# Performance work log

Hardware: AMD Instinct MI355X
Metric: run time of the kernel (lower is better)

Reference implementation:

```python
import jax, jax.numpy as jnp
import numpy as np

N, E = 50000, 800000
H, C, K = 8, 16, 4
LAMBD = 1.0
DECAY = [float(np.log(LAMBD / (k + 1) + (1 + 1e-06))) for k in range(K + 1)]


def setup_inputs() -> dict:
    key = jax.random.key(0)
    ks = jax.random.split(key, 10)
    s = 0.05  # keep activations stable over K hops
    return {
        "x": jax.random.normal(ks[0], (N, 256), jnp.float32),
        "edge_index": jax.random.randint(ks[1], (2, E), 0, N, jnp.int64),
        "W0": jax.random.normal(ks[2], (256, 128), jnp.float32) * s,
        "b0": jnp.zeros((128,), jnp.float32),
        "W1": jax.random.normal(ks[3], (128, 128), jnp.float32) * s,
        "b1": jnp.zeros((128,), jnp.float32),
        "Wout": jax.random.normal(ks[4], (128, 40), jnp.float32) * s,
        "bout": jnp.zeros((40,), jnp.float32),
        "hop_att0": jax.random.normal(ks[5], (H, C), jnp.float32) * s,
        "hop_atts": jax.random.normal(ks[6], (K, H, 2 * C), jnp.float32) * s,
        "atts": jax.random.normal(ks[7], (K, H, C), jnp.float32) * s,
        "hop_biases": jnp.ones((K + 1, H), jnp.float32),
    }


def _aero_forward(x, edge_index, W0, b0, W1, b1, Wout, bout,
                  hop_att0, hop_atts, atts, hop_biases):
    n = x.shape[0]
    # add self loops (cached_edge_index is None in the torch module)
    loops = jnp.arange(n, dtype=edge_index.dtype)
    row = jnp.concatenate([edge_index[0], loops])  # source j
    col = jnp.concatenate([edge_index[1], loops])  # target i

    # hid_feat_init (dropout p=0 -> identity); num_layers=2
    h = x @ W0 + b0
    h = jax.nn.elu(h) @ W1 + b1
    h = h.reshape(n, H, C)

    # k = 0 hop attention
    g = jnp.einsum('hc,nhc->nh', hop_att0, jax.nn.elu(h)) + hop_biases[0]
    z = h * g[..., None]
    z_scale = z * DECAY[0]

    for k in range(1, K + 1):
        # edge attention: gather, elementwise, degree-normalize
        zi = z_scale[col]          # [E', H, C] target
        zj = z_scale[row]          # [E', H, C] source
        a = jnp.einsum('hc,ehc->eh', atts[k - 1], jax.nn.elu(zi + zj))
        a = jax.nn.softplus(a) + 1e-06                       # [E', H]
        deg = jax.ops.segment_sum(a, col, num_segments=n)    # [N, H]
        dinv = jnp.where(deg > 0, deg ** -0.5, 0.0)
        a = dinv[row] * a * dinv[col]
        # propagate: scatter-add weighted source features onto targets
        h = jax.ops.segment_sum(a[..., None] * h[row], col, num_segments=n)
        # hop attention on concat(h, z_scale)
        hz = jax.nn.elu(jnp.concatenate([h, z_scale], axis=-1))  # [N, H, 2C]
        g = jnp.einsum('hc,nhc->nh', hop_atts[k - 1], hz) + hop_biases[k]
        z = z + h * g[..., None]
        z_scale = z * DECAY[k]

    # node classifier
    z = jax.nn.elu(z.reshape(n, H * C))
    return z @ Wout + bout


def reference(x, edge_index, W0, b0, W1, b1, Wout, bout,
              hop_att0, hop_atts, atts, hop_biases):
    return _aero_forward(x, edge_index, W0, b0, W1, b1, Wout, bout,
                         hop_att0, hop_atts, atts, hop_biases)
```

## Files before the change

kernel.cpp:

```cpp
#include <hip/hip_runtime.h>
#include <hip/hip_fp16.h>
#include <math.h>

#define NH 8
#define NC 16
#define HC 128

typedef __attribute__((ext_vector_type(8))) _Float16 half8;
typedef __attribute__((ext_vector_type(4))) float f32x4;

__device__ __forceinline__ float eluf(float x) { return x > 0.f ? x : __expf(x) - 1.f; }
__device__ __forceinline__ float splusf(float x) { return fmaxf(x, 0.f) + __logf(1.f + __expf(-fabsf(x))); }

#if __has_builtin(__builtin_amdgcn_exp2f)
#define EXP2F(x) __builtin_amdgcn_exp2f(x)
#else
#define EXP2F(x) exp2f(x)
#endif

__global__ void count_kernel(const int* __restrict__ ei, int* __restrict__ cnt, int E, int E2) {
    int e = blockIdx.x * blockDim.x + threadIdx.x;
    if (e >= E2) return;
    int col = (e < E) ? ei[E + e] : (e - E);
    atomicAdd(&cnt[col], 1);
}

__global__ void scan1_kernel(const int* __restrict__ counts, int* __restrict__ ptr,
                             int* __restrict__ partials, int n) {
    __shared__ int tmp[256];
    int t = threadIdx.x;
    int i = blockIdx.x * 256 + t;
    int v = (i < n) ? counts[i] : 0;
    tmp[t] = v;
    __syncthreads();
    for (int off = 1; off < 256; off <<= 1) {
        int add = (t >= off) ? tmp[t - off] : 0;
        __syncthreads();
        tmp[t] += add;
        __syncthreads();
    }
    if (i < n) ptr[i] = tmp[t] - v;
    if (t == 255) partials[blockIdx.x] = tmp[255];
}

__global__ void scan2_kernel(int* __restrict__ partials, int nb) {
    __shared__ int tmp[256];
    int t = threadIdx.x;
    int v = (t < nb) ? partials[t] : 0;
    tmp[t] = v;
    __syncthreads();
    for (int off = 1; off < 256; off <<= 1) {
        int add = (t >= off) ? tmp[t - off] : 0;
        __syncthreads();
        tmp[t] += add;
        __syncthreads();
    }
    if (t < nb) partials[t] = tmp[t] - v;
}

__global__ void scan3_kernel(int* __restrict__ ptr, const int* __restrict__ partials,
                             int n, int total) {
    int i = blockIdx.x * 256 + threadIdx.x;
    if (i < n) ptr[i] += partials[blockIdx.x];
    if (i == 0) ptr[n] = total;
}

__global__ void fill_kernel(const int* __restrict__ ei, const int* __restrict__ ptr,
                            int* __restrict__ cursor, int* __restrict__ src, int E, int E2) {
    int e = blockIdx.x * blockDim.x + threadIdx.x;
    if (e >= E2) return;
    int col, row;
    if (e < E) { row = ei[e]; col = ei[E + e]; }
    else       { row = e - E; col = e - E; }
    int pos = ptr[col] + atomicAdd(&cursor[col], 1);
    src[pos] = row;
}

__global__ void wswz_kernel(const float* __restrict__ W, _Float16* __restrict__ Wf, int NKS) {
    int t = blockIdx.x * 256 + threadIdx.x;
    if (t >= 8 * NKS * 64) return;
    int lane = t & 63;
    int ks = (t >> 6) % NKS;
    int cg = (t >> 6) / NKS;
    int n = cg * 16 + (lane & 15);
    int k0 = ks * 32 + (lane >> 4) * 8;
    half8 v;
#pragma unroll
    for (int j = 0; j < 8; ++j) v[j] = (_Float16)W[(size_t)(k0 + j) * 128 + n];
    *(half8*)(Wf + (size_t)t * 8) = v;
}

template<int K, bool A16, bool HOP0>
__global__ __launch_bounds__(256)
void mfma_gemm(const float* __restrict__ A32, const _Float16* __restrict__ A16p,
               const _Float16* __restrict__ Wf, const float* __restrict__ bias,
               int M, _Float16* __restrict__ h1_out,
               float* __restrict__ z_out, _Float16* __restrict__ h16_out,
               _Float16* __restrict__ z16_out,
               const float* __restrict__ att0, const float* __restrict__ hb0) {
    constexpr int NKS = K / 32;
    __shared__ float sL[64 * 132];
    const int tid = threadIdx.x;
    const int w = tid >> 6;
    const int lane = tid & 63;
    const int l15 = lane & 15;
    const int lg = lane >> 4;
    const int m0 = blockIdx.x * 64;

    f32x4 acc[4][2];
#pragma unroll
    for (int a = 0; a < 4; ++a)
#pragma unroll
        for (int b = 0; b < 2; ++b)
            acc[a][b] = f32x4{0.f, 0.f, 0.f, 0.f};

#pragma unroll
    for (int ks = 0; ks < NKS; ++ks) {
        const int kb = ks * 32 + lg * 8;
        half8 af[4];
        if (A16) {
#pragma unroll
            for (int mf = 0; mf < 4; ++mf) {
                int row = m0 + mf * 16 + l15;
                af[mf] = *(const half8*)(A16p + ((size_t)row << 7) + kb);
            }
        } else {
#pragma unroll
            for (int mf = 0; mf < 4; ++mf) {
                int row = m0 + mf * 16 + l15;
                float4 a0 = make_float4(0.f, 0.f, 0.f, 0.f), a1 = a0;
                if (row < M) {
                    const float* ap = A32 + (size_t)row * K + kb;
                    a0 = *(const float4*)ap;
                    a1 = *(const float4*)(ap + 4);
                }
                half8 h;
                h[0] = (_Float16)a0.x; h[1] = (_Float16)a0.y;
                h[2] = (_Float16)a0.z; h[3] = (_Float16)a0.w;
                h[4] = (_Float16)a1.x; h[5] = (_Float16)a1.y;
                h[6] = (_Float16)a1.z; h[7] = (_Float16)a1.w;
                af[mf] = h;
            }
        }
        half8 bf[2];
#pragma unroll
        for (int cf = 0; cf < 2; ++cf) {
            int cg = w * 2 + cf;
            bf[cf] = *(const half8*)(Wf + (size_t)((cg * NKS + ks) * 64 + lane) * 8);
        }
#pragma unroll
        for (int mf = 0; mf < 4; ++mf)
#pragma unroll
            for (int cf = 0; cf < 2; ++cf)
                acc[mf][cf] = __builtin_amdgcn_mfma_f32_16x16x32_f16(af[mf], bf[cf],
                                                                     acc[mf][cf], 0, 0, 0);
    }

#pragma unroll
    for (int mf = 0; mf < 4; ++mf)
#pragma unroll
        for (int cf = 0; cf < 2; ++cf) {
            int col = w * 32 + cf * 16 + l15;
#pragma unroll
            for (int r = 0; r < 4; ++r)
                sL[(mf * 16 + lg * 4 + r) * 132 + col] = acc[mf][cf][r];
        }
    __syncthreads();

    const int rr = lane;
    const int q = w;
    const int row = m0 + rr;
    float v[32];
#pragma unroll
    for (int t = 0; t < 8; ++t)
        *(float4*)&v[t * 4] = *(const float4*)&sL[rr * 132 + q * 32 + t * 4];
#pragma unroll
    for (int t = 0; t < 8; ++t) {
        float4 bv = *(const float4*)&bias[q * 32 + t * 4];
        v[t * 4 + 0] += bv.x; v[t * 4 + 1] += bv.y;
        v[t * 4 + 2] += bv.z; v[t * 4 + 3] += bv.w;
    }

    if (!HOP0) {
        if (row < M) {
            half8 o[4];
#pragma unroll
            for (int c = 0; c < 32; ++c) o[c >> 3][c & 7] = (_Float16)eluf(v[c]);
            _Float16* hp = h1_out + ((size_t)row << 7) + q * 32;
#pragma unroll
            for (int t = 0; t < 4; ++t) *(half8*)(hp + t * 8) = o[t];
        }
    } else {
        float g[2];
#pragma unroll
        for (int hh = 0; hh < 2; ++hh) {
            int head = q * 2 + hh;
            float p = 0.f;
#pragma unroll
            for (int c = 0; c < 16; ++c)
                p = fmaf(att0[head * 16 + c], eluf(v[hh * 16 + c]), p);
            g[hh] = p + hb0[head];
        }
        if (row < M) {
            float zz[32];
#pragma unroll
            for (int c = 0; c < 32; ++c) zz[c] = v[c] * g[c >> 4];
            half8 ho[4], zo[4];
#pragma unroll
            for (int c = 0; c < 32; ++c) {
                ho[c >> 3][c & 7] = (_Float16)v[c];
                zo[c >> 3][c & 7] = (_Float16)zz[c];
            }
            _Float16* hp  = h16_out + ((size_t)row << 7) + q * 32;
            _Float16* zhp = z16_out + ((size_t)row << 7) + q * 32;
            float*    zp  = z_out   + ((size_t)row << 7) + q * 32;
#pragma unroll
            for (int t = 0; t < 4; ++t) {
                *(half8*)(hp + t * 8) = ho[t];
                *(half8*)(zhp + t * 8) = zo[t];
            }
#pragma unroll
            for (int t = 0; t < 8; ++t)
                *(float4*)(zp + t * 4) = make_float4(zz[t * 4 + 0], zz[t * 4 + 1],
                                                     zz[t * 4 + 2], zz[t * 4 + 3]);
        }
    }
}

__global__ __launch_bounds__(256)
void passA_kernel(const _Float16* __restrict__ z16, const int* __restrict__ ptr,
                  const int* __restrict__ src, const float* __restrict__ att,
                  float decay, _Float16* __restrict__ a_e, float* __restrict__ dinv, int n) {
    int wid = (int)((blockIdx.x * 256u + threadIdx.x) >> 6);
    if (wid >= n) return;
    const int lane = threadIdx.x & 63;
    const int g  = lane >> 4;
    const int q  = lane & 15;
    const int hd = q >> 1;
    const unsigned i = (unsigned)wid;
    const float dl2 = decay * 1.44269504089f;

    float ziL[8];
    {
        const half8 zi = *(const half8*)(z16 + ((size_t)i << 7) + (q << 3));
#pragma unroll
        for (int c = 0; c < 8; ++c) ziL[c] = (float)zi[c] * dl2;
    }
    float av[8];
    *(float4*)&av[0] = *(const float4*)(att + (q << 3));
    *(float4*)&av[4] = *(const float4*)(att + (q << 3) + 4);
    float sav = ((av[0] + av[1]) + (av[2] + av[3]))
              + ((av[4] + av[5]) + (av[6] + av[7]));
    sav += __shfl_xor(sav, 1);

    const int s0 = ptr[wid], s1 = ptr[wid + 1];
    float dacc = 0.f;

#define PA_BODY(f, sv) do {                                                  \
        float pm = 0.f, pe = 0.f;                                            \
        _Pragma("unroll")                                                    \
        for (int c = 0; c < 8; ++c) {                                        \
            float y = fmaf((float)(f)[c], dl2, ziL[c]);                      \
            float e2 = EXP2F(fminf(y, 0.f));                                 \
            pm = fmaf(av[c], fmaxf(y, 0.f), pm);                             \
            pe = fmaf(av[c], e2, pe);                                        \
        }                                                                    \
        float pc = fmaf(pm, 0.69314718056f, pe);                             \
        pc += __shfl_xor(pc, 1);                                             \
        if ((q & 1) == 0) {                                                  \
            float aval = splusf(pc - sav) + 1e-6f;                           \
            a_e[((size_t)(sv) << 3) + hd] = (_Float16)aval;                  \
            dacc += aval;                                                    \
        }                                                                    \
    } while (0)

    const int nfull = (s1 - s0) & ~7;
    const int send = s0 + nfull;
    for (int s = s0 + g; s < send; s += 8) {
        unsigned ja = (unsigned)src[s];
        unsigned jb = (unsigned)src[s + 4];
        const half8 fa = *(const half8*)(z16 + ((size_t)ja << 7) + (q << 3));
        const half8 fb = *(const half8*)(z16 + ((size_t)jb << 7) + (q << 3));
        PA_BODY(fa, s);
        PA_BODY(fb, s + 4);
    }
    {
        int sA = send + g;
        if (sA < s1) {
            unsigned ja = (unsigned)src[sA];
            const half8 fa = *(const half8*)(z16 + ((size_t)ja << 7) + (q << 3));
            PA_BODY(fa, sA);
        }
        int sB = send + 4 + g;
        if (sB < s1) {
            unsigned jb = (unsigned)src[sB];
            const half8 fb = *(const half8*)(z16 + ((size_t)jb << 7) + (q << 3));
            PA_BODY(fb, sB);
        }
    }
#undef PA_BODY

    dacc += __shfl_xor(dacc, 16);
    dacc += __shfl_xor(dacc, 32);
    if ((lane & 0x31) == 0) {
        dinv[((size_t)i << 3) + hd] = (dacc > 0.f) ? (1.f / sqrtf(dacc)) : 0.f;
    }
}

__global__ __launch_bounds__(256)
void passB_kernel(const _Float16* __restrict__ h_in, float* __restrict__ z,
                  _Float16* __restrict__ z16,
                  const int* __restrict__ ptr, const int* __restrict__ src,
                  const _Float16* __restrict__ a_e, const float* __restrict__ dinv,
                  const float* __restrict__ hatt, const float* __restrict__ hb,
                  float decay, _Float16* __restrict__ h_out, int n, int store_h) {
    int wid = (int)((blockIdx.x * 256u + threadIdx.x) >> 6);
    if (wid >= n) return;
    const int lane = threadIdx.x & 63;
    const int g  = lane >> 4;
    const int q  = lane & 15;
    const int hd = q >> 1;
    const unsigned i = (unsigned)wid;

    const float di = dinv[((size_t)i << 3) + hd];
    const int s0 = ptr[wid], s1 = ptr[wid + 1];
    float acc[8];
#pragma unroll
    for (int c = 0; c < 8; ++c) acc[c] = 0.f;

    const int nfull = (s1 - s0) & ~7;
    const int send = s0 + nfull;
    for (int s = s0 + g; s < send; s += 8) {
        unsigned ja = (unsigned)src[s];
        unsigned jb = (unsigned)src[s + 4];
        const _Float16 aA = a_e[((size_t)s << 3) + hd];
        const _Float16 aB = a_e[((size_t)(s + 4) << 3) + hd];
        const float dA = dinv[((size_t)ja << 3) + hd];
        const float dB = dinv[((size_t)jb << 3) + hd];
        const half8 fa = *(const half8*)(h_in + ((size_t)ja << 7) + (q << 3));
        const half8 fb = *(const half8*)(h_in + ((size_t)jb << 7) + (q << 3));
        const float wa = (float)aA * dA;
        const float wb = (float)aB * dB;
#pragma unroll
        for (int c = 0; c < 8; ++c) acc[c] = fmaf((float)fa[c], wa, acc[c]);
#pragma unroll
        for (int c = 0; c < 8; ++c) acc[c] = fmaf((float)fb[c], wb, acc[c]);
    }
    {
        int sA = send + g;
        if (sA < s1) {
            unsigned j = (unsigned)src[sA];
            const float w = (float)a_e[((size_t)sA << 3) + hd] * dinv[((size_t)j << 3) + hd];
            const half8 f = *(const half8*)(h_in + ((size_t)j << 7) + (q << 3));
#pragma unroll
            for (int c = 0; c < 8; ++c) acc[c] = fmaf((float)f[c], w, acc[c]);
        }
        int sB = send + 4 + g;
        if (sB < s1) {
            unsigned j = (unsigned)src[sB];
            const float w = (float)a_e[((size_t)sB << 3) + hd] * dinv[((size_t)j << 3) + hd];
            const half8 f = *(const half8*)(h_in + ((size_t)j << 7) + (q << 3));
#pragma unroll
            for (int c = 0; c < 8; ++c) acc[c] = fmaf((float)f[c], w, acc[c]);
        }
    }
#pragma unroll
    for (int c = 0; c < 8; ++c) {
        acc[c] += __shfl_xor(acc[c], 16);
        acc[c] += __shfl_xor(acc[c], 32);
    }

    float hn[8];
#pragma unroll
    for (int c = 0; c < 8; ++c) hn[c] = di * acc[c];

    float* zrow = z + ((size_t)i << 7) + (q << 3);
    const float4 zva = *(const float4*)zrow;
    const float4 zvb = *(const float4*)(zrow + 4);
    float zv[8] = {zva.x, zva.y, zva.z, zva.w, zvb.x, zvb.y, zvb.z, zvb.w};

    const float* hA = hatt + hd * 32 + (q & 1) * 8;
    float p = 0.f;
#pragma unroll
    for (int c = 0; c < 8; ++c) p = fmaf(hA[c], eluf(hn[c]), p);
#pragma unroll
    for (int c = 0; c < 8; ++c) p = fmaf(hA[16 + c], eluf(zv[c] * decay), p);
    p += __shfl_xor(p, 1);
    const float gv = p + hb[hd];

    if (g == 0) {
        float zn[8];
#pragma unroll
        for (int c = 0; c < 8; ++c) zn[c] = fmaf(hn[c], gv, zv[c]);
        *(float4*)zrow       = make_float4(zn[0], zn[1], zn[2], zn[3]);
        *(float4*)(zrow + 4) = make_float4(zn[4], zn[5], zn[6], zn[7]);
        if (store_h) {
            half8 ho, zo;
#pragma unroll
            for (int c = 0; c < 8; ++c) { ho[c] = (_Float16)hn[c]; zo[c] = (_Float16)zn[c]; }
            *(half8*)(h_out + ((size_t)i << 7) + (q << 3)) = ho;
            *(half8*)(z16   + ((size_t)i << 7) + (q << 3)) = zo;
        }
    }
}

__global__ __launch_bounds__(256)
void gout_kernel(const float* __restrict__ z, const float* __restrict__ W,
                 const float* __restrict__ bias, float* __restrict__ out, int M) {
    __shared__ float zs[128 * 65];
    __shared__ float ws[128 * 40];
    const int tid = threadIdx.x;
    const int r0 = blockIdx.x * 64;
    for (int idx = tid; idx < 128 * 40; idx += 256) ws[idx] = W[idx];
    const int r = tid >> 2;
    const int q = tid & 3;
    {
        int grow = r0 + r;
#pragma unroll
        for (int t = 0; t < 8; ++t) {
            int k = q * 4 + t * 16;
            float4 v = make_float4(0.f, 0.f, 0.f, 0.f);
            if (grow < M) v = *(const float4*)(z + (size_t)grow * HC + k);
            zs[(k + 0) * 65 + r] = eluf(v.x);
            zs[(k + 1) * 65 + r] = eluf(v.y);
            zs[(k + 2) * 65 + r] = eluf(v.z);
            zs[(k + 3) * 65 + r] = eluf(v.w);
        }
    }
    __syncthreads();
    float acc[10];
#pragma unroll
    for (int j = 0; j < 10; ++j) acc[j] = bias[q * 10 + j];
    for (int k = 0; k < 128; ++k) {
        float zk = zs[k * 65 + r];
#pragma unroll
        for (int j = 0; j < 10; ++j)
            acc[j] = fmaf(zk, ws[k * 40 + q * 10 + j], acc[j]);
    }
    int grow = r0 + r;
    if (grow < M) {
        float* op = out + (size_t)grow * 40 + q * 10;
#pragma unroll
        for (int j = 0; j < 10; ++j) op[j] = acc[j];
    }
}

extern "C" void kernel_launch(void* const* d_in, const int* in_sizes, int n_in,
                              void* d_out, int out_size, void* d_ws, size_t ws_size,
                              hipStream_t stream) {
    (void)n_in; (void)out_size; (void)ws_size;
    const float* x    = (const float*)d_in[0];
    const int*   ei   = (const int*)d_in[1];
    const float* W0   = (const float*)d_in[2];
    const float* b0   = (const float*)d_in[3];
    const float* W1   = (const float*)d_in[4];
    const float* b1   = (const float*)d_in[5];
    const float* Wout = (const float*)d_in[6];
    const float* bout = (const float*)d_in[7];
    const float* att0 = (const float*)d_in[8];
    const float* hatts= (const float*)d_in[9];
    const float* atts = (const float*)d_in[10];
    const float* hb   = (const float*)d_in[11];
    float* out = (float*)d_out;

    const int N  = in_sizes[0] / 256;
    const int E  = in_sizes[1] / 2;
    const int E2 = E + N;
    const size_t Npad = ((size_t)N + 63) & ~(size_t)63;

    char* p = (char*)d_ws;
    auto carve = [&](size_t bytes) -> char* {
        char* r = p;
        p += (bytes + 255) & ~(size_t)255;
        return r;
    };
    _Float16* h1     = (_Float16*)carve(Npad * HC * 2);
    _Float16* hbufA  = (_Float16*)carve((size_t)N * HC * 2);
    _Float16* hbufB  = (_Float16*)carve((size_t)N * HC * 2);
    float*    zbuf   = (float*)carve((size_t)N * HC * 4);
    _Float16* z16buf = (_Float16*)carve((size_t)N * HC * 2);
    _Float16* a_e    = (_Float16*)carve((size_t)E2 * NH * 2);
    float*    dinvb  = (float*)carve((size_t)N * NH * 4);
    _Float16* Wf0    = (_Float16*)carve((size_t)8 * 8 * 64 * 8 * 2);
    _Float16* Wf1    = (_Float16*)carve((size_t)8 * 4 * 64 * 8 * 2);
    int* csr_ptr   = (int*)carve((size_t)(N + 1) * 4);
    int* csr_src   = (int*)carve((size_t)E2 * 4);
    int* cursor    = (int*)carve((size_t)N * 4);
    int* partials  = (int*)carve(1024 * 4);

    float decay[5];
    for (int k = 0; k <= 4; ++k) decay[k] = (float)log(1.0 / (k + 1) + 1.0 + 1e-6);

    hipMemsetAsync(cursor, 0, (size_t)N * 4, stream);
    int eb = (E2 + 255) / 256;
    int nb = (N + 255) / 256;
    count_kernel<<<eb, 256, 0, stream>>>(ei, cursor, E, E2);
    scan1_kernel<<<nb, 256, 0, stream>>>(cursor, csr_ptr, partials, N);
    scan2_kernel<<<1, 256, 0, stream>>>(partials, nb);
    scan3_kernel<<<nb, 256, 0, stream>>>(csr_ptr, partials, N, E2);
    hipMemsetAsync(cursor, 0, (size_t)N * 4, stream);
    fill_kernel<<<eb, 256, 0, stream>>>(ei, csr_ptr, cursor, csr_src, E, E2);

    wswz_kernel<<<16, 256, 0, stream>>>(W0, Wf0, 8);
    wswz_kernel<<<8, 256, 0, stream>>>(W1, Wf1, 4);

    int gb = (N + 63) / 64;
    mfma_gemm<256, false, false><<<gb, 256, 0, stream>>>(
        x, nullptr, Wf0, b0, N, h1, nullptr, nullptr, nullptr, nullptr, nullptr);
    mfma_gemm<128, true, true><<<gb, 256, 0, stream>>>(
        nullptr, h1, Wf1, b1, N, nullptr, zbuf, hbufA, z16buf, att0, hb);

    _Float16* hin  = hbufA;
    _Float16* hout = hbufB;
    int wb = (N + 3) / 4;
    for (int k = 1; k <= 4; ++k) {
        passA_kernel<<<wb, 256, 0, stream>>>(z16buf, csr_ptr, csr_src,
                                             atts + (size_t)(k - 1) * NH * NC,
                                             decay[k - 1], a_e, dinvb, N);
        passB_kernel<<<wb, 256, 0, stream>>>(hin, zbuf, z16buf, csr_ptr, csr_src,
                                             a_e, dinvb,
                                             hatts + (size_t)(k - 1) * NH * 32,
                                             hb + (size_t)k * NH, decay[k - 1], hout, N,
                                             (k < 4) ? 1 : 0);
        _Float16* t = hin; hin = hout; hout = t;
    }

    gout_kernel<<<(N + 63) / 64, 256, 0, stream>>>(zbuf, Wout, bout, out, N);
}
```

Before: 670.7 us.

## Build CSR via bucketed shared-memory sort and add nontemporal memory hints

Replaces the count/scan/fill CSR construction (per-node global atomics, five launches plus memsets) with a two-pass bucket sort: edges are binned into 256-node buckets with block-local histograms, then each bucket is sorted in shared memory to emit row pointers and sources. Scratch pairs reuse the z buffer. Separately, streaming loads and stores in the propagation and classifier kernels are marked nontemporal to reduce cache pollution. Buckets have a fixed capacity, so highly skewed degree distributions would be truncated.

```diff
diff --git a/kernel.cpp b/kernel.cpp
--- a/kernel.cpp
+++ b/kernel.cpp
@@ -5,6 +5,7 @@
 #define NH 8
 #define NC 16
 #define HC 128
+#define CAPB 12288
 
 typedef __attribute__((ext_vector_type(8))) _Float16 half8;
 typedef __attribute__((ext_vector_type(4))) float f32x4;
@@ -18,19 +19,54 @@
 #define EXP2F(x) exp2f(x)
 #endif
 
-__global__ void count_kernel(const int* __restrict__ ei, int* __restrict__ cnt, int E, int E2) {
-    int e = blockIdx.x * blockDim.x + threadIdx.x;
-    if (e >= E2) return;
-    int col = (e < E) ? ei[E + e] : (e - E);
-    atomicAdd(&cnt[col], 1);
-}
-
-__global__ void scan1_kernel(const int* __restrict__ counts, int* __restrict__ ptr,
-                             int* __restrict__ partials, int n) {
+template <typename T>
+__device__ __forceinline__ T ntload(const T* p) { return __builtin_nontemporal_load(p); }
+template <typename T>
+__device__ __forceinline__ void ntstore(T* p, T v) { __builtin_nontemporal_store(v, p); }
+
+__global__ __launch_bounds__(256)
+void csr1_kernel(const int* __restrict__ ei, uint2* __restrict__ pairs,
+                 int* __restrict__ gCnt, int E, int E2) {
+    __shared__ int h1[256];
+    __shared__ int bbase[256];
+    __shared__ int cur[256];
+    const int t = threadIdx.x;
+    const int e0 = blockIdx.x * 4096;
+    int rows[16], cols[16];
+#pragma unroll
+    for (int i = 0; i < 16; ++i) {
+        int e = e0 + i * 256 + t;
+        int r = 0, c = -1;
+        if (e < E) { r = ei[e]; c = ei[E + e]; }
+        else if (e < E2) { r = e - E; c = e - E; }
+        rows[i] = r; cols[i] = c;
+    }
+    h1[t] = 0; cur[t] = 0;
+    __syncthreads();
+#pragma unroll
+    for (int i = 0; i < 16; ++i)
+        if (cols[i] >= 0) atomicAdd(&h1[cols[i] >> 8], 1);
+    __syncthreads();
+    if (h1[t] > 0) bbase[t] = atomicAdd(&gCnt[t], h1[t]);
+    __syncthreads();
+#pragma unroll
+    for (int i = 0; i < 16; ++i) {
+        if (cols[i] >= 0) {
+            int b = cols[i] >> 8;
+            int r = atomicAdd(&cur[b], 1);
+            int pos = bbase[b] + r;
+            if (pos < CAPB)
+                pairs[(size_t)b * CAPB + pos] =
+                    make_uint2((unsigned)rows[i], (unsigned)cols[i]);
+        }
+    }
+}
+
+__global__ void scanbkt_kernel(const int* __restrict__ gCnt, int* __restrict__ bktPtr,
+                               int NBKT) {
     __shared__ int tmp[256];
     int t = threadIdx.x;
-    int i = blockIdx.x * 256 + t;
-    int v = (i < n) ? counts[i] : 0;
+    int v = (t < NBKT) ? gCnt[t] : 0;
     tmp[t] = v;
     __syncthreads();
     for (int off = 1; off < 256; off <<= 1) {
@@ -39,41 +75,55 @@
         tmp[t] += add;
         __syncthreads();
     }
-    if (i < n) ptr[i] = tmp[t] - v;
-    if (t == 255) partials[blockIdx.x] = tmp[255];
-}
-
-__global__ void scan2_kernel(int* __restrict__ partials, int nb) {
-    __shared__ int tmp[256];
-    int t = threadIdx.x;
-    int v = (t < nb) ? partials[t] : 0;
-    tmp[t] = v;
+    if (t < NBKT) bktPtr[t] = tmp[t] - v;
+}
+
+__global__ __launch_bounds__(256)
+void csr2_kernel(const uint2* __restrict__ pairs, const int* __restrict__ gCnt,
+                 const int* __restrict__ bktPtr, int* __restrict__ ptr,
+                 int* __restrict__ src, int N, int NBKT, int E2) {
+    __shared__ int hist[256];
+    __shared__ int scanb[256];
+    __shared__ int cur[256];
+    __shared__ int stage[CAPB];
+    const int b = blockIdx.x;
+    const int t = threadIdx.x;
+    const int c0 = b << 8;
+    int cnt = gCnt[b]; if (cnt > CAPB) cnt = CAPB;
+    const int base = bktPtr[b];
+    hist[t] = 0; cur[t] = 0;
+    __syncthreads();
+    const uint2* bp = pairs + (size_t)b * CAPB;
+    for (int idx = t; idx < cnt; idx += 256) {
+        int c = (int)bp[idx].y - c0;
+        atomicAdd(&hist[c], 1);
+    }
+    __syncthreads();
+    int v = hist[t];
+    scanb[t] = v;
     __syncthreads();
     for (int off = 1; off < 256; off <<= 1) {
-        int add = (t >= off) ? tmp[t - off] : 0;
+        int add = (t >= off) ? scanb[t - off] : 0;
         __syncthreads();
-        tmp[t] += add;
+        scanb[t] += add;
         __syncthreads();
     }
-    if (t < nb) partials[t] = tmp[t] - v;
-}
-
-__global__ void scan3_kernel(int* __restrict__ ptr, const int* __restrict__ partials,
-                             int n, int total) {
-    int i = blockIdx.x * 256 + threadIdx.x;
-    if (i < n) ptr[i] += partials[blockIdx.x];
-    if (i == 0) ptr[n] = total;
-}
-
-__global__ void fill_kernel(const int* __restrict__ ei, const int* __restrict__ ptr,
-                            int* __restrict__ cursor, int* __restrict__ src, int E, int E2) {
-    int e = blockIdx.x * blockDim.x + threadIdx.x;
-    if (e >= E2) return;
-    int col, row;
-    if (e < E) { row = ei[e]; col = ei[E + e]; }
-    else       { row = e - E; col = e - E; }
-    int pos = ptr[col] + atomicAdd(&cursor[col], 1);
-    src[pos] = row;
+    int excl = scanb[t] - v;
+    int ncols = N - c0; if (ncols > 256) ncols = 256;
+    if (t < ncols) ptr[c0 + t] = base + excl;
+    if (b == NBKT - 1 && t == 0) ptr[N] = E2;
+    __syncthreads();
+    scanb[t] = excl;
+    __syncthreads();
+    for (int idx = t; idx < cnt; idx += 256) {
+        uint2 u = bp[idx];
+        int c = (int)u.y - c0;
+        int r = atomicAdd(&cur[c], 1);
+        stage[scanb[c] + r] = (int)u.x;
+    }
+    __syncthreads();
+    for (int idx = t; idx < cnt; idx += 256)
+        ntstore(&src[base + idx], stage[idx]);
 }
 
 __global__ void wswz_kernel(const float* __restrict__ W, _Float16* __restrict__ Wf, int NKS) {
@@ -269,7 +319,7 @@
         pc += __shfl_xor(pc, 1);                                             \
         if ((q & 1) == 0) {                                                  \
             float aval = splusf(pc - sav) + 1e-6f;                           \
-            a_e[((size_t)(sv) << 3) + hd] = (_Float16)aval;                  \
+            ntstore(&a_e[((size_t)(sv) << 3) + hd], (_Float16)aval);         \
             dacc += aval;                                                    \
         }                                                                    \
     } while (0)
@@ -277,8 +327,8 @@
     const int nfull = (s1 - s0) & ~7;
     const int send = s0 + nfull;
     for (int s = s0 + g; s < send; s += 8) {
-        unsigned ja = (unsigned)src[s];
-        unsigned jb = (unsigned)src[s + 4];
+        unsigned ja = (unsigned)ntload(&src[s]);
+        unsigned jb = (unsigned)ntload(&src[s + 4]);
         const half8 fa = *(const half8*)(z16 + ((size_t)ja << 7) + (q << 3));
         const half8 fb = *(const half8*)(z16 + ((size_t)jb << 7) + (q << 3));
         PA_BODY(fa, s);
@@ -331,10 +381,10 @@
     const int nfull = (s1 - s0) & ~7;
     const int send = s0 + nfull;
     for (int s = s0 + g; s < send; s += 8) {
-        unsigned ja = (unsigned)src[s];
-        unsigned jb = (unsigned)src[s + 4];
-        const _Float16 aA = a_e[((size_t)s << 3) + hd];
-        const _Float16 aB = a_e[((size_t)(s + 4) << 3) + hd];
+        unsigned ja = (unsigned)ntload(&src[s]);
+        unsigned jb = (unsigned)ntload(&src[s + 4]);
+        const _Float16 aA = ntload(&a_e[((size_t)s << 3) + hd]);
+        const _Float16 aB = ntload(&a_e[((size_t)(s + 4) << 3) + hd]);
         const float dA = dinv[((size_t)ja << 3) + hd];
         const float dB = dinv[((size_t)jb << 3) + hd];
         const half8 fa = *(const half8*)(h_in + ((size_t)ja << 7) + (q << 3));
@@ -375,8 +425,8 @@
     for (int c = 0; c < 8; ++c) hn[c] = di * acc[c];
 
     float* zrow = z + ((size_t)i << 7) + (q << 3);
-    const float4 zva = *(const float4*)zrow;
-    const float4 zvb = *(const float4*)(zrow + 4);
+    const f32x4 zva = ntload((const f32x4*)zrow);
+    const f32x4 zvb = ntload((const f32x4*)(zrow + 4));
     float zv[8] = {zva.x, zva.y, zva.z, zva.w, zvb.x, zvb.y, zvb.z, zvb.w};
 
     const float* hA = hatt + hd * 32 + (q & 1) * 8;
@@ -392,14 +442,14 @@
         float zn[8];
 #pragma unroll
         for (int c = 0; c < 8; ++c) zn[c] = fmaf(hn[c], gv, zv[c]);
-        *(float4*)zrow       = make_float4(zn[0], zn[1], zn[2], zn[3]);
-        *(float4*)(zrow + 4) = make_float4(zn[4], zn[5], zn[6], zn[7]);
+        ntstore((f32x4*)zrow, f32x4{zn[0], zn[1], zn[2], zn[3]});
+        ntstore((f32x4*)(zrow + 4), f32x4{zn[4], zn[5], zn[6], zn[7]});
         if (store_h) {
             half8 ho, zo;
 #pragma unroll
             for (int c = 0; c < 8; ++c) { ho[c] = (_Float16)hn[c]; zo[c] = (_Float16)zn[c]; }
-            *(half8*)(h_out + ((size_t)i << 7) + (q << 3)) = ho;
-            *(half8*)(z16   + ((size_t)i << 7) + (q << 3)) = zo;
+            ntstore((half8*)(h_out + ((size_t)i << 7) + (q << 3)), ho);
+            ntstore((half8*)(z16   + ((size_t)i << 7) + (q << 3)), zo);
         }
     }
 }
@@ -419,8 +469,8 @@
 #pragma unroll
         for (int t = 0; t < 8; ++t) {
             int k = q * 4 + t * 16;
-            float4 v = make_float4(0.f, 0.f, 0.f, 0.f);
-            if (grow < M) v = *(const float4*)(z + (size_t)grow * HC + k);
+            f32x4 v = f32x4{0.f, 0.f, 0.f, 0.f};
+            if (grow < M) v = ntload((const f32x4*)(z + (size_t)grow * HC + k));
             zs[(k + 0) * 65 + r] = eluf(v.x);
             zs[(k + 1) * 65 + r] = eluf(v.y);
             zs[(k + 2) * 65 + r] = eluf(v.z);
@@ -466,6 +516,7 @@
     const int N  = in_sizes[0] / 256;
     const int E  = in_sizes[1] / 2;
     const int E2 = E + N;
+    const int NBKT = (N + 255) >> 8;
     const size_t Npad = ((size_t)N + 63) & ~(size_t)63;
 
     char* p = (char*)d_ws;
@@ -485,21 +536,19 @@
     _Float16* Wf1    = (_Float16*)carve((size_t)8 * 4 * 64 * 8 * 2);
     int* csr_ptr   = (int*)carve((size_t)(N + 1) * 4);
     int* csr_src   = (int*)carve((size_t)E2 * 4);
-    int* cursor    = (int*)carve((size_t)N * 4);
-    int* partials  = (int*)carve(1024 * 4);
+    int* gCnt      = (int*)carve(256 * 4);
+    int* bktPtr    = (int*)carve(257 * 4);
+    uint2* pairs = (uint2*)zbuf;
 
     float decay[5];
     for (int k = 0; k <= 4; ++k) decay[k] = (float)log(1.0 / (k + 1) + 1.0 + 1e-6);
 
-    hipMemsetAsync(cursor, 0, (size_t)N * 4, stream);
-    int eb = (E2 + 255) / 256;
-    int nb = (N + 255) / 256;
-    count_kernel<<<eb, 256, 0, stream>>>(ei, cursor, E, E2);
-    scan1_kernel<<<nb, 256, 0, stream>>>(cursor, csr_ptr, partials, N);
-    scan2_kernel<<<1, 256, 0, stream>>>(partials, nb);
-    scan3_kernel<<<nb, 256, 0, stream>>>(csr_ptr, partials, N, E2);
-    hipMemsetAsync(cursor, 0, (size_t)N * 4, stream);
-    fill_kernel<<<eb, 256, 0, stream>>>(ei, csr_ptr, cursor, csr_src, E, E2);
+    hipMemsetAsync(gCnt, 0, 256 * 4, stream);
+    int b1n = (E2 + 4095) / 4096;
+    csr1_kernel<<<b1n, 256, 0, stream>>>(ei, pairs, gCnt, E, E2);
+    scanbkt_kernel<<<1, 256, 0, stream>>>(gCnt, bktPtr, NBKT);
+    csr2_kernel<<<NBKT, 256, 0, stream>>>(pairs, gCnt, bktPtr, csr_ptr, csr_src,
+                                          N, NBKT, E2);
 
     wswz_kernel<<<16, 256, 0, stream>>>(W0, Wf0, 8);
     wswz_kernel<<<8, 256, 0, stream>>>(W1, Wf1, 4);
```

Result: faster. 638.2 us (-4.9%).
